# Performance work log

Measured on AMD Instinct MI355X. Metric: run time of the kernel, lower is better.

Reference implementation:

```python
import jax, jax.numpy as jnp
import numpy as np
import math

B, T, C = 8, 2048, 1024
N_LAYER, LAYER_ID = 24, 12


def setup_inputs() -> dict:
    key = jax.random.key(0)
    ks = jax.random.split(key, 8)
    # deterministic parameter init, mirroring RWKV_TimeMix.__init__
    ratio_0_to_1 = LAYER_ID / (N_LAYER - 1)
    ratio_1_to_almost0 = 1.0 - LAYER_ID / N_LAYER
    h = np.arange(C, dtype=np.float64)
    time_decay = (-5 + 8 * (h / (C - 1)) ** (0.7 + 1.3 * ratio_0_to_1)).astype(np.float32)
    zigzag = (np.array([(i + 1) % 3 - 1 for i in range(C)], dtype=np.float64) * 0.5)
    time_first = (np.ones(C) * math.log(0.3) + zigzag).astype(np.float32)
    xpos = (np.arange(C, dtype=np.float64) / C)
    time_mix_k = (xpos ** ratio_1_to_almost0).astype(np.float32).reshape(1, 1, C)
    time_mix_v = (xpos ** ratio_1_to_almost0 + 0.3 * ratio_0_to_1).astype(np.float32).reshape(1, 1, C)
    time_mix_r = (xpos ** (0.5 * ratio_1_to_almost0)).astype(np.float32).reshape(1, 1, C)
    scale = 1.0 / math.sqrt(C)
    return {
        "x": jax.random.normal(ks[0], (B, T, C), jnp.float32),
        "time_decay": jnp.asarray(time_decay),
        "time_first": jnp.asarray(time_first),
        "time_mix_k": jnp.asarray(time_mix_k),
        "time_mix_v": jnp.asarray(time_mix_v),
        "time_mix_r": jnp.asarray(time_mix_r),
        "Wk": jax.random.normal(ks[1], (C, C), jnp.float32) * scale,
        "Wv": jax.random.normal(ks[2], (C, C), jnp.float32) * scale,
        "Wr": jax.random.normal(ks[3], (C, C), jnp.float32) * scale,
        "Wo": jax.random.normal(ks[4], (C, C), jnp.float32) * scale,
    }


def wkv_scan(w_decay, u, k, v):
    """Numerically-stable RWKV-4 WKV recurrence.
    w_decay, u: [C]; k, v: [B, T, C]. Returns [B, T, C].
    """
    w = -jnp.exp(w_decay)  # negative decay per channel
    kt = jnp.swapaxes(k, 0, 1)  # [T, B, C]
    vt = jnp.swapaxes(v, 0, 1)
    Bn, Cn = k.shape[0], k.shape[2]
    aa0 = jnp.zeros((Bn, Cn), k.dtype)
    bb0 = jnp.zeros((Bn, Cn), k.dtype)
    pp0 = jnp.full((Bn, Cn), -1e38, k.dtype)

    def step(carry, kv):
        aa, bb, pp = carry
        k_t, v_t = kv
        ww = u + k_t
        q = jnp.maximum(pp, ww)
        e1 = jnp.exp(pp - q)
        e2 = jnp.exp(ww - q)
        y = (e1 * aa + e2 * v_t) / (e1 * bb + e2)
        ww2 = pp + w
        q2 = jnp.maximum(ww2, k_t)
        e1 = jnp.exp(ww2 - q2)
        e2 = jnp.exp(k_t - q2)
        return (e1 * aa + e2 * v_t, e1 * bb + e2, q2), y

    _, ys = jax.lax.scan(step, (aa0, bb0, pp0), (kt, vt))
    return jnp.swapaxes(ys, 0, 1)  # [B, T, C]


def reference(x, time_decay, time_first, time_mix_k, time_mix_v, time_mix_r, Wk, Wv, Wr, Wo):
    # time shift: x_{t-1}, zero at t=0
    xx = jnp.pad(x, ((0, 0), (1, 0), (0, 0)))[:, :-1]
    xk = x * time_mix_k + xx * (1.0 - time_mix_k)
    xv = x * time_mix_v + xx * (1.0 - time_mix_v)
    xr = x * time_mix_r + xx * (1.0 - time_mix_r)
    k = jnp.einsum("btc,oc->bto", xk, Wk)
    v = jnp.einsum("btc,oc->bto", xv, Wv)
    r = jnp.einsum("btc,oc->bto", xr, Wr)
    wkv = wkv_scan(time_decay, time_first, k, v)
    rwkv = jax.nn.sigmoid(r) * wkv
    return jnp.einsum("btc,oc->bto", rwkv, Wo)
```

## Files before the change

### kernel.cpp

```cpp
#include <hip/hip_runtime.h>

#define BB 8
#define TT 2048
#define CC 1024
#define WKV_L 32
#define WKV_NCH (TT / WKV_L)
#define WKV_LOG_NCH 6

typedef __bf16 bf16x8_t __attribute__((ext_vector_type(8)));
typedef float f32x4_t __attribute__((ext_vector_type(4)));

__device__ __forceinline__ unsigned short f2bf(float f) {
  unsigned u = __float_as_uint(f);
  u += 0x7fffu + ((u >> 16) & 1u);
  return (unsigned short)(u >> 16);
}
__device__ __forceinline__ float bf2f(unsigned short s) {
  return __uint_as_float(((unsigned)s) << 16);
}

#define GLOAD16(gp, lp)                                                        \
  __builtin_amdgcn_global_load_lds(                                            \
      (const __attribute__((address_space(1))) void*)(gp),                     \
      (__attribute__((address_space(3))) void*)(lp), 16, 0, 0)

__global__ __launch_bounds__(256) void mix3_cast_kernel(
    const float* __restrict__ x, const float* __restrict__ tmk,
    const float* __restrict__ tmv, const float* __restrict__ tmr,
    unsigned short* __restrict__ xk, unsigned short* __restrict__ xv,
    unsigned short* __restrict__ xr) {
  const size_t total4 = (size_t)BB * TT * CC / 4;
  for (size_t i = (size_t)blockIdx.x * blockDim.x + threadIdx.x; i < total4;
       i += (size_t)gridDim.x * blockDim.x) {
    size_t e = i * 4;
    int c = (int)(e & (CC - 1));
    int t = (int)((e / CC) & (TT - 1));
    float4 xv4 = ((const float4*)x)[i];
    float4 xp = make_float4(0.f, 0.f, 0.f, 0.f);
    if (t > 0) xp = ((const float4*)x)[i - CC / 4];
    float4 mk = *(const float4*)(tmk + c);
    float4 mv = *(const float4*)(tmv + c);
    float4 mr = *(const float4*)(tmr + c);
    ushort4 ok, ov, orr;
    ok.x = f2bf(xv4.x * mk.x + xp.x * (1.f - mk.x));
    ok.y = f2bf(xv4.y * mk.y + xp.y * (1.f - mk.y));
    ok.z = f2bf(xv4.z * mk.z + xp.z * (1.f - mk.z));
    ok.w = f2bf(xv4.w * mk.w + xp.w * (1.f - mk.w));
    ov.x = f2bf(xv4.x * mv.x + xp.x * (1.f - mv.x));
    ov.y = f2bf(xv4.y * mv.y + xp.y * (1.f - mv.y));
    ov.z = f2bf(xv4.z * mv.z + xp.z * (1.f - mv.z));
    ov.w = f2bf(xv4.w * mv.w + xp.w * (1.f - mv.w));
    orr.x = f2bf(xv4.x * mr.x + xp.x * (1.f - mr.x));
    orr.y = f2bf(xv4.y * mr.y + xp.y * (1.f - mr.y));
    orr.z = f2bf(xv4.z * mr.z + xp.z * (1.f - mr.z));
    orr.w = f2bf(xv4.w * mr.w + xp.w * (1.f - mr.w));
    *(ushort4*)(xk + e) = ok;
    *(ushort4*)(xv + e) = ov;
    *(ushort4*)(xr + e) = orr;
  }
}

__global__ __launch_bounds__(256) void cast_w4_kernel(
    const float* __restrict__ w0, const float* __restrict__ w1,
    const float* __restrict__ w2, const float* __restrict__ w3,
    unsigned short* __restrict__ o0, unsigned short* __restrict__ o1,
    unsigned short* __restrict__ o2, unsigned short* __restrict__ o3) {
  const int n4 = CC * CC / 4;
  for (int i = blockIdx.x * blockDim.x + threadIdx.x; i < 4 * n4;
       i += gridDim.x * blockDim.x) {
    int sel = i / n4;
    int j = i - sel * n4;
    const float* w = sel == 0 ? w0 : sel == 1 ? w1 : sel == 2 ? w2 : w3;
    unsigned short* o = sel == 0 ? o0 : sel == 1 ? o1 : sel == 2 ? o2 : o3;
    float4 v = ((const float4*)w)[j];
    ushort4 u;
    u.x = f2bf(v.x); u.y = f2bf(v.y); u.z = f2bf(v.z); u.w = f2bf(v.w);
    ((ushort4*)o)[j] = u;
  }
}

#define NT8 (CC / 64)

template <typename EPI>
__device__ __forceinline__ void gemm8_body(unsigned short* lds8,
                                           const unsigned short* __restrict__ A,
                                           const unsigned short* __restrict__ Bm,
                                           int tm, int tn, EPI epi) {
  const int tid = threadIdx.x;
  const int lane = tid & 63;
  const int wid = tid >> 6;
  const int wr = wid >> 2;
  const int wc = wid & 3;
  const int fr = lane & 15;
  const int fk = lane >> 4;

  const int srow = tid >> 3;
  const int gcol = (((tid & 7) ^ (srow & 7)) << 3);
  const unsigned short* Ag = A + (size_t)(tm * 256 + srow) * CC + gcol;
  const unsigned short* Bg = Bm + (size_t)(tn * 256 + srow) * CC + gcol;
  const int ldst = tid << 3;

  const int rowA = wr * 16 + fr;
  const int rowB = wc * 16 + fr;
  const int sx0 = ((fk ^ (fr & 7)) << 3);
  const int sx1 = (((4 + fk) ^ (fr & 7)) << 3);

  bf16x8_t aF[4][2];
  bf16x8_t bF[2][2][2];
  f32x4_t acc[8][4] = {};

#define STG_A(T, H)                                                            \
  {                                                                            \
    const unsigned short* g_ = Ag + (size_t)((H) * 128) * CC + (T) * 64;       \
    unsigned short* l_ = &lds8[(((T) & 1) << 14) + (H) * 8192 + ldst];         \
    GLOAD16(g_, l_);                                                           \
    GLOAD16(g_ + (size_t)64 * CC, l_ + 4096);                                  \
  }
#define STG_B(T, H)                                                            \
  {                                                                            \
    const unsigned short* g_ = Bg + (size_t)((H) * 128) * CC + (T) * 64;       \
    unsigned short* l_ = &lds8[32768 + (((T) & 1) << 14) + (H) * 8192 + ldst]; \
    GLOAD16(g_, l_);                                                           \
    GLOAD16(g_ + (size_t)64 * CC, l_ + 4096);                                  \
  }
#define LOADA(MH)                                                              \
  _Pragma("unroll") for (int i_ = 0; i_ < 4; ++i_) {                           \
    aF[i_][0] = *(const bf16x8_t*)&lds8[ab + ((MH) * 4 + i_) * 2048 + sx0];    \
    aF[i_][1] = *(const bf16x8_t*)&lds8[ab + ((MH) * 4 + i_) * 2048 + sx1];    \
  }
#define LOADB(NH)                                                              \
  _Pragma("unroll") for (int j_ = 0; j_ < 2; ++j_) {                           \
    bF[NH][j_][0] = *(const bf16x8_t*)&lds8[bb + ((NH) * 2 + j_) * 4096 + sx0];\
    bF[NH][j_][1] = *(const bf16x8_t*)&lds8[bb + ((NH) * 2 + j_) * 4096 + sx1];\
  }
#define MFMAQ(MH, NH)                                                          \
  _Pragma("unroll") for (int i_ = 0; i_ < 4; ++i_)                             \
  _Pragma("unroll") for (int j_ = 0; j_ < 2; ++j_) {                           \
    acc[(MH) * 4 + i_][(NH) * 2 + j_] = __builtin_amdgcn_mfma_f32_16x16x32_bf16( \
        aF[i_][0], bF[NH][j_][0], acc[(MH) * 4 + i_][(NH) * 2 + j_], 0, 0, 0); \
    acc[(MH) * 4 + i_][(NH) * 2 + j_] = __builtin_amdgcn_mfma_f32_16x16x32_bf16( \
        aF[i_][1], bF[NH][j_][1], acc[(MH) * 4 + i_][(NH) * 2 + j_], 0, 0, 0); \
  }

  STG_A(0, 0) STG_B(0, 0) STG_A(0, 1) STG_B(0, 1)
  STG_A(1, 0) STG_B(1, 0) STG_A(1, 1)
  asm volatile("s_waitcnt vmcnt(10)" ::: "memory");
  __builtin_amdgcn_s_barrier();

#pragma unroll
  for (int t = 0; t < NT8; ++t) {
    const int ab = ((t & 1) << 14) + rowA * 64;
    const int bb = 32768 + ((t & 1) << 14) + rowB * 64;
    LOADA(0) LOADB(0)
    if (t + 1 < NT8) { STG_B(t + 1, 1) }
    asm volatile("s_waitcnt vmcnt(8)" ::: "memory");
    __builtin_amdgcn_s_barrier();
    __builtin_amdgcn_s_setprio(1);
    MFMAQ(0, 0)
    __builtin_amdgcn_s_setprio(0);
    __builtin_amdgcn_s_barrier();
    LOADB(1)
    if (t + 2 < NT8) { STG_A(t + 2, 0) }
    __builtin_amdgcn_s_barrier();
    __builtin_amdgcn_s_setprio(1);
    MFMAQ(0, 1)
    __builtin_amdgcn_s_setprio(0);
    __builtin_amdgcn_s_barrier();
    LOADA(1)
    if (t + 2 < NT8) { STG_B(t + 2, 0) }
    __builtin_amdgcn_s_barrier();
    __builtin_amdgcn_s_setprio(1);
    MFMAQ(1, 0)
    __builtin_amdgcn_s_setprio(0);
    __builtin_amdgcn_s_barrier();
    if (t + 2 < NT8) { STG_A(t + 2, 1) }
    asm volatile("s_waitcnt vmcnt(10)" ::: "memory");
    __builtin_amdgcn_s_barrier();
    __builtin_amdgcn_s_setprio(1);
    MFMAQ(1, 1)
    __builtin_amdgcn_s_setprio(0);
    __builtin_amdgcn_s_barrier();
  }

#pragma unroll
  for (int im = 0; im < 8; ++im)
#pragma unroll
    for (int jn = 0; jn < 4; ++jn)
#pragma unroll
      for (int rg = 0; rg < 4; ++rg)
        epi((size_t)(tm * 256 + wr * 16 + im * 32 + (fk << 2) + rg) * CC +
                (size_t)(tn * 256 + wc * 16 + jn * 64 + fr),
            acc[im][jn][rg]);
#undef STG_A
#undef STG_B
#undef LOADA
#undef LOADB
#undef MFMAQ
}

template <int OUT_BF16>
__global__ __launch_bounds__(512, 2) void gemm8_one(const unsigned short* __restrict__ A,
                         const unsigned short* __restrict__ Bm,
                         void* __restrict__ Cm) {
  __shared__ unsigned short lds8[65536];
  int orig = blockIdx.x;
  int wg = (orig & 7) * 32 + (orig >> 3);
  int tm = wg >> 2;
  int tn = wg & 3;
  if (OUT_BF16)
    gemm8_body(lds8, A, Bm, tm, tn,
               [&](size_t off, float val) { ((unsigned short*)Cm)[off] = f2bf(val); });
  else
    gemm8_body(lds8, A, Bm, tm, tn,
               [&](size_t off, float val) { ((float*)Cm)[off] = val; });
}

__global__ __launch_bounds__(256) void wkv_phase1(const float* __restrict__ k,
                           const unsigned short* __restrict__ v,
                           const float* __restrict__ wdec,
                           float* __restrict__ Sa, float* __restrict__ Sb,
                           float* __restrict__ Sp) {
  int idx = blockIdx.x * blockDim.x + threadIdx.x;
  int c = idx & (CC - 1);
  int bj = idx >> 10;
  int j = bj & (WKV_NCH - 1);
  int b = bj >> WKV_LOG_NCH;
  float w = -__expf(wdec[c]);
  size_t base = ((size_t)b * TT + (size_t)j * WKV_L) * CC + c;
  float aa = 0.f, bb = 0.f, pp = -1e38f;
  for (int t = 0; t < WKV_L; ++t) {
    size_t off = base + (size_t)t * CC;
    float kt = k[off];
    float vt = bf2f(v[off]);
    pp += w;
    float d = kt - pp;
    if (d > 8.f) {
      float s = __expf(-d);
      aa *= s; bb *= s; pp = kt; d = 0.f;
    }
    float E = __expf(d);
    aa = fmaf(E, vt, aa);
    bb += E;
  }
  Sa[idx] = aa; Sb[idx] = bb; Sp[idx] = pp;
}

__global__ __launch_bounds__(256) void wkv_phase2(const float* __restrict__ wdec,
                           const float* __restrict__ Sa, const float* __restrict__ Sb,
                           const float* __restrict__ Sp,
                           float* __restrict__ Ia, float* __restrict__ Ib,
                           float* __restrict__ Ip) {
  int idx = blockIdx.x * blockDim.x + threadIdx.x;
  if (idx >= BB * CC) return;
  int c = idx & (CC - 1);
  int b = idx >> 10;
  float wL = -__expf(wdec[c]) * (float)WKV_L;
  float aa = 0.f, bb = 0.f, pp = -1e38f;
  for (int j = 0; j < WKV_NCH; ++j) {
    size_t s = (size_t)(b * WKV_NCH + j) * CC + c;
    Ia[s] = aa; Ib[s] = bb; Ip[s] = pp;
    float pd = pp + wL;
    float ps = Sp[s];
    float q = fmaxf(pd, ps);
    float e1 = __expf(pd - q);
    float e2 = __expf(ps - q);
    aa = fmaf(e1, aa, e2 * Sa[s]);
    bb = fmaf(e1, bb, e2 * Sb[s]);
    pp = q;
  }
}

__global__ __launch_bounds__(256) void wkv_phase3(const float* __restrict__ k,
                           const unsigned short* __restrict__ v,
                           const unsigned short* r,
                           const float* __restrict__ wdec,
                           const float* __restrict__ u,
                           const float* __restrict__ Ia, const float* __restrict__ Ib,
                           const float* __restrict__ Ip,
                           unsigned short* out) {
  int idx = blockIdx.x * blockDim.x + threadIdx.x;
  int c = idx & (CC - 1);
  int bj = idx >> 10;
  int j = bj & (WKV_NCH - 1);
  int b = bj >> WKV_LOG_NCH;
  float w = -__expf(wdec[c]);
  float uu = u[c];
  float aa = Ia[idx], bb = Ib[idx], pp = Ip[idx];
  size_t base = ((size_t)b * TT + (size_t)j * WKV_L) * CC + c;
  for (int t = 0; t < WKV_L; ++t) {
    size_t off = base + (size_t)t * CC;
    float kt = k[off];
    float vt = bf2f(v[off]);
    float dy = fminf(uu + kt - pp, 60.f);
    float Eu = __expf(dy);
    float y = fmaf(Eu, vt, aa) / (bb + Eu);
    float rt = bf2f(r[off]);
    float sr = 1.f / (1.f + __expf(-rt));
    out[off] = f2bf(sr * y);
    pp += w;
    float d = kt - pp;
    if (d > 8.f) {
      float s = __expf(-d);
      aa *= s; bb *= s; pp = kt; d = 0.f;
    }
    float E = __expf(d);
    aa = fmaf(E, vt, aa);
    bb += E;
  }
}

extern "C" void kernel_launch(void* const* d_in, const int* in_sizes, int n_in,
                              void* d_out, int out_size, void* d_ws, size_t ws_size,
                              hipStream_t stream) {
  const float* x    = (const float*)d_in[0];
  const float* tdec = (const float*)d_in[1];
  const float* tfir = (const float*)d_in[2];
  const float* tmk  = (const float*)d_in[3];
  const float* tmv  = (const float*)d_in[4];
  const float* tmr  = (const float*)d_in[5];
  const float* Wk   = (const float*)d_in[6];
  const float* Wv   = (const float*)d_in[7];
  const float* Wr   = (const float*)d_in[8];
  const float* Wo   = (const float*)d_in[9];

  const size_t M = (size_t)BB * TT;
  const size_t mixbytes = M * CC * 2;
  const size_t wbytes = (size_t)CC * CC * 2;
  const size_t nstate = (size_t)BB * WKV_NCH * CC;

  char* ws = (char*)d_ws;
  unsigned short* xkb = (unsigned short*)ws;  ws += mixbytes;
  unsigned short* xvb = (unsigned short*)ws;  ws += mixbytes;
  unsigned short* xrb = (unsigned short*)ws;  ws += mixbytes;
  unsigned short* rbuf = xkb;
  unsigned short* Wkb = (unsigned short*)ws; ws += wbytes;
  unsigned short* Wvb = (unsigned short*)ws; ws += wbytes;
  unsigned short* Wrb = (unsigned short*)ws; ws += wbytes;
  unsigned short* Wob = (unsigned short*)ws; ws += wbytes;
  float* kbuf = (float*)ws;                   ws += M * CC * 4;
  unsigned short* vbuf = (unsigned short*)ws; ws += mixbytes;
  float* Sa = (float*)ws; ws += nstate * 4;
  float* Sb = (float*)ws; ws += nstate * 4;
  float* Sp = (float*)ws; ws += nstate * 4;
  float* Ia = (float*)ws; ws += nstate * 4;
  float* Ib = (float*)ws; ws += nstate * 4;
  float* Ip = (float*)ws; ws += nstate * 4;

  dim3 blk(256);
  dim3 blk8(512);
  const int wkv_grid = (int)(nstate / 256);

  cast_w4_kernel<<<1024, blk, 0, stream>>>(Wk, Wv, Wr, Wo, Wkb, Wvb, Wrb, Wob);
  mix3_cast_kernel<<<2048, blk, 0, stream>>>(x, tmk, tmv, tmr, xkb, xvb, xrb);
  gemm8_one<0><<<256, blk8, 0, stream>>>(xkb, Wkb, kbuf);
  gemm8_one<1><<<256, blk8, 0, stream>>>(xvb, Wvb, vbuf);
  gemm8_one<1><<<256, blk8, 0, stream>>>(xrb, Wrb, rbuf);

  wkv_phase1<<<wkv_grid, blk, 0, stream>>>(kbuf, vbuf, tdec, Sa, Sb, Sp);
  wkv_phase2<<<(BB * CC + 255) / 256, blk, 0, stream>>>(tdec, Sa, Sb, Sp, Ia, Ib, Ip);
  wkv_phase3<<<wkv_grid, blk, 0, stream>>>(kbuf, vbuf, rbuf, tdec, tfir,
                                           Ia, Ib, Ip, rbuf);

  gemm8_one<0><<<256, blk8, 0, stream>>>(rbuf, Wob, d_out);
}
```

Baseline: 258.7 us.

## Batch K/V/R GEMMs into one launch, store k in bf16, vectorize WKV

Merges the three projection GEMMs into one grouped kernel with 768 workgroups so the CUs hold more concurrent blocks. It stores k as bf16 instead of fp32, which lowers memory traffic for the WKV phases. The WKV kernels now process two channels per thread with paired loads and stores, and the mixing kernel handles 8 elements per thread. The WKV state buffers reuse the no-longer-needed xk workspace. The trade-offs are less k precision and a possible wave-tail imbalance in the grouped GEMM.

```diff
diff --git a/kernel.cpp b/kernel.cpp
--- a/kernel.cpp
+++ b/kernel.cpp
@@ -9,6 +9,7 @@
 
 typedef __bf16 bf16x8_t __attribute__((ext_vector_type(8)));
 typedef float f32x4_t __attribute__((ext_vector_type(4)));
+typedef unsigned short ushort8_t __attribute__((ext_vector_type(8)));
 
 __device__ __forceinline__ unsigned short f2bf(float f) {
   unsigned u = __float_as_uint(f);
@@ -29,34 +30,41 @@
     const float* __restrict__ tmv, const float* __restrict__ tmr,
     unsigned short* __restrict__ xk, unsigned short* __restrict__ xv,
     unsigned short* __restrict__ xr) {
-  const size_t total4 = (size_t)BB * TT * CC / 4;
-  for (size_t i = (size_t)blockIdx.x * blockDim.x + threadIdx.x; i < total4;
+  const size_t total8 = (size_t)BB * TT * CC / 8;
+  for (size_t i = (size_t)blockIdx.x * blockDim.x + threadIdx.x; i < total8;
        i += (size_t)gridDim.x * blockDim.x) {
-    size_t e = i * 4;
+    size_t e = i * 8;
     int c = (int)(e & (CC - 1));
     int t = (int)((e / CC) & (TT - 1));
-    float4 xv4 = ((const float4*)x)[i];
-    float4 xp = make_float4(0.f, 0.f, 0.f, 0.f);
-    if (t > 0) xp = ((const float4*)x)[i - CC / 4];
-    float4 mk = *(const float4*)(tmk + c);
-    float4 mv = *(const float4*)(tmv + c);
-    float4 mr = *(const float4*)(tmr + c);
-    ushort4 ok, ov, orr;
-    ok.x = f2bf(xv4.x * mk.x + xp.x * (1.f - mk.x));
-    ok.y = f2bf(xv4.y * mk.y + xp.y * (1.f - mk.y));
-    ok.z = f2bf(xv4.z * mk.z + xp.z * (1.f - mk.z));
-    ok.w = f2bf(xv4.w * mk.w + xp.w * (1.f - mk.w));
-    ov.x = f2bf(xv4.x * mv.x + xp.x * (1.f - mv.x));
-    ov.y = f2bf(xv4.y * mv.y + xp.y * (1.f - mv.y));
-    ov.z = f2bf(xv4.z * mv.z + xp.z * (1.f - mv.z));
-    ov.w = f2bf(xv4.w * mv.w + xp.w * (1.f - mv.w));
-    orr.x = f2bf(xv4.x * mr.x + xp.x * (1.f - mr.x));
-    orr.y = f2bf(xv4.y * mr.y + xp.y * (1.f - mr.y));
-    orr.z = f2bf(xv4.z * mr.z + xp.z * (1.f - mr.z));
-    orr.w = f2bf(xv4.w * mr.w + xp.w * (1.f - mr.w));
-    *(ushort4*)(xk + e) = ok;
-    *(ushort4*)(xv + e) = ov;
-    *(ushort4*)(xr + e) = orr;
+    float4 xa = ((const float4*)x)[2 * i];
+    float4 xb = ((const float4*)x)[2 * i + 1];
+    float4 pa = make_float4(0.f, 0.f, 0.f, 0.f), pb = pa;
+    if (t > 0) {
+      pa = ((const float4*)x)[2 * i - 256];
+      pb = ((const float4*)x)[2 * i - 255];
+    }
+    float4 mka = *(const float4*)(tmk + c), mkb = *(const float4*)(tmk + c + 4);
+    float4 mva = *(const float4*)(tmv + c), mvb = *(const float4*)(tmv + c + 4);
+    float4 mra = *(const float4*)(tmr + c), mrb = *(const float4*)(tmr + c + 4);
+    ushort8_t ok, ov, orr;
+#define MIX1(dst, idx, xv_, pv_, m_)                                           \
+    dst[idx] = f2bf(xv_ * m_ + pv_ * (1.f - m_));
+    MIX1(ok, 0, xa.x, pa.x, mka.x) MIX1(ok, 1, xa.y, pa.y, mka.y)
+    MIX1(ok, 2, xa.z, pa.z, mka.z) MIX1(ok, 3, xa.w, pa.w, mka.w)
+    MIX1(ok, 4, xb.x, pb.x, mkb.x) MIX1(ok, 5, xb.y, pb.y, mkb.y)
+    MIX1(ok, 6, xb.z, pb.z, mkb.z) MIX1(ok, 7, xb.w, pb.w, mkb.w)
+    MIX1(ov, 0, xa.x, pa.x, mva.x) MIX1(ov, 1, xa.y, pa.y, mva.y)
+    MIX1(ov, 2, xa.z, pa.z, mva.z) MIX1(ov, 3, xa.w, pa.w, mva.w)
+    MIX1(ov, 4, xb.x, pb.x, mvb.x) MIX1(ov, 5, xb.y, pb.y, mvb.y)
+    MIX1(ov, 6, xb.z, pb.z, mvb.z) MIX1(ov, 7, xb.w, pb.w, mvb.w)
+    MIX1(orr, 0, xa.x, pa.x, mra.x) MIX1(orr, 1, xa.y, pa.y, mra.y)
+    MIX1(orr, 2, xa.z, pa.z, mra.z) MIX1(orr, 3, xa.w, pa.w, mra.w)
+    MIX1(orr, 4, xb.x, pb.x, mrb.x) MIX1(orr, 5, xb.y, pb.y, mrb.y)
+    MIX1(orr, 6, xb.z, pb.z, mrb.z) MIX1(orr, 7, xb.w, pb.w, mrb.w)
+#undef MIX1
+    *(ushort8_t*)(xk + e) = ok;
+    *(ushort8_t*)(xv + e) = ov;
+    *(ushort8_t*)(xr + e) = orr;
   }
 }
 
@@ -198,51 +206,70 @@
 #undef MFMAQ
 }
 
-template <int OUT_BF16>
+__global__ __launch_bounds__(512, 2) void gemm8_kvr(
+    const unsigned short* __restrict__ xk, const unsigned short* __restrict__ xv,
+    const unsigned short* __restrict__ xr, const unsigned short* __restrict__ Wk,
+    const unsigned short* __restrict__ Wv, const unsigned short* __restrict__ Wr,
+    unsigned short* __restrict__ kout, unsigned short* __restrict__ vout,
+    unsigned short* __restrict__ rout) {
+  __shared__ unsigned short lds8[65536];
+  int orig = blockIdx.x;
+  int wg = (orig & 7) * 96 + (orig >> 3);
+  int which = wg >> 8;
+  int rr = wg & 255;
+  int tm = rr >> 2;
+  int tn = rr & 3;
+  const unsigned short* A = which == 0 ? xk : which == 1 ? xv : xr;
+  const unsigned short* Bm = which == 0 ? Wk : which == 1 ? Wv : Wr;
+  unsigned short* o = which == 0 ? kout : which == 1 ? vout : rout;
+  gemm8_body(lds8, A, Bm, tm, tn,
+             [&](size_t off, float val) { o[off] = f2bf(val); });
+}
+
 __global__ __launch_bounds__(512, 2) void gemm8_one(const unsigned short* __restrict__ A,
                          const unsigned short* __restrict__ Bm,
-                         void* __restrict__ Cm) {
+                         float* __restrict__ Cm) {
   __shared__ unsigned short lds8[65536];
   int orig = blockIdx.x;
   int wg = (orig & 7) * 32 + (orig >> 3);
   int tm = wg >> 2;
   int tn = wg & 3;
-  if (OUT_BF16)
-    gemm8_body(lds8, A, Bm, tm, tn,
-               [&](size_t off, float val) { ((unsigned short*)Cm)[off] = f2bf(val); });
-  else
-    gemm8_body(lds8, A, Bm, tm, tn,
-               [&](size_t off, float val) { ((float*)Cm)[off] = val; });
-}
-
-__global__ __launch_bounds__(256) void wkv_phase1(const float* __restrict__ k,
+  gemm8_body(lds8, A, Bm, tm, tn,
+             [&](size_t off, float val) { Cm[off] = val; });
+}
+
+__global__ __launch_bounds__(256) void wkv_phase1(const unsigned short* __restrict__ k,
                            const unsigned short* __restrict__ v,
                            const float* __restrict__ wdec,
                            float* __restrict__ Sa, float* __restrict__ Sb,
                            float* __restrict__ Sp) {
   int idx = blockIdx.x * blockDim.x + threadIdx.x;
-  int c = idx & (CC - 1);
-  int bj = idx >> 10;
+  int c = (idx & (CC / 2 - 1)) << 1;
+  int bj = idx >> 9;
   int j = bj & (WKV_NCH - 1);
   int b = bj >> WKV_LOG_NCH;
-  float w = -__expf(wdec[c]);
+  float w0 = -__expf(wdec[c]), w1 = -__expf(wdec[c + 1]);
   size_t base = ((size_t)b * TT + (size_t)j * WKV_L) * CC + c;
-  float aa = 0.f, bb = 0.f, pp = -1e38f;
+  float aa0 = 0.f, bb0 = 0.f, pp0 = -1e38f;
+  float aa1 = 0.f, bb1 = 0.f, pp1 = -1e38f;
   for (int t = 0; t < WKV_L; ++t) {
     size_t off = base + (size_t)t * CC;
-    float kt = k[off];
-    float vt = bf2f(v[off]);
-    pp += w;
-    float d = kt - pp;
-    if (d > 8.f) {
-      float s = __expf(-d);
-      aa *= s; bb *= s; pp = kt; d = 0.f;
-    }
-    float E = __expf(d);
-    aa = fmaf(E, vt, aa);
-    bb += E;
-  }
-  Sa[idx] = aa; Sb[idx] = bb; Sp[idx] = pp;
+    ushort2 kk = *(const ushort2*)(k + off);
+    ushort2 vv = *(const ushort2*)(v + off);
+    float k0 = bf2f(kk.x), k1 = bf2f(kk.y);
+    float v0 = bf2f(vv.x), v1 = bf2f(vv.y);
+    pp0 += w0; pp1 += w1;
+    float d0 = k0 - pp0, d1 = k1 - pp1;
+    if (d0 > 8.f) { float s = __expf(-d0); aa0 *= s; bb0 *= s; pp0 = k0; d0 = 0.f; }
+    if (d1 > 8.f) { float s = __expf(-d1); aa1 *= s; bb1 *= s; pp1 = k1; d1 = 0.f; }
+    float E0 = __expf(d0), E1 = __expf(d1);
+    aa0 = fmaf(E0, v0, aa0); bb0 += E0;
+    aa1 = fmaf(E1, v1, aa1); bb1 += E1;
+  }
+  size_t s = (size_t)bj * CC + c;
+  *(float2*)(Sa + s) = make_float2(aa0, aa1);
+  *(float2*)(Sb + s) = make_float2(bb0, bb1);
+  *(float2*)(Sp + s) = make_float2(pp0, pp1);
 }
 
 __global__ __launch_bounds__(256) void wkv_phase2(const float* __restrict__ wdec,
@@ -270,7 +297,7 @@
   }
 }
 
-__global__ __launch_bounds__(256) void wkv_phase3(const float* __restrict__ k,
+__global__ __launch_bounds__(256) void wkv_phase3(const unsigned short* __restrict__ k,
                            const unsigned short* __restrict__ v,
                            const unsigned short* r,
                            const float* __restrict__ wdec,
@@ -279,33 +306,44 @@
                            const float* __restrict__ Ip,
                            unsigned short* out) {
   int idx = blockIdx.x * blockDim.x + threadIdx.x;
-  int c = idx & (CC - 1);
-  int bj = idx >> 10;
+  int c = (idx & (CC / 2 - 1)) << 1;
+  int bj = idx >> 9;
   int j = bj & (WKV_NCH - 1);
   int b = bj >> WKV_LOG_NCH;
-  float w = -__expf(wdec[c]);
-  float uu = u[c];
-  float aa = Ia[idx], bb = Ib[idx], pp = Ip[idx];
+  float w0 = -__expf(wdec[c]), w1 = -__expf(wdec[c + 1]);
+  float u0 = u[c], u1 = u[c + 1];
+  size_t st = (size_t)bj * CC + c;
+  float2 a2 = *(const float2*)(Ia + st);
+  float2 b2 = *(const float2*)(Ib + st);
+  float2 p2 = *(const float2*)(Ip + st);
+  float aa0 = a2.x, bb0 = b2.x, pp0 = p2.x;
+  float aa1 = a2.y, bb1 = b2.y, pp1 = p2.y;
   size_t base = ((size_t)b * TT + (size_t)j * WKV_L) * CC + c;
   for (int t = 0; t < WKV_L; ++t) {
     size_t off = base + (size_t)t * CC;
-    float kt = k[off];
-    float vt = bf2f(v[off]);
-    float dy = fminf(uu + kt - pp, 60.f);
-    float Eu = __expf(dy);
-    float y = fmaf(Eu, vt, aa) / (bb + Eu);
-    float rt = bf2f(r[off]);
-    float sr = 1.f / (1.f + __expf(-rt));
-    out[off] = f2bf(sr * y);
-    pp += w;
-    float d = kt - pp;
-    if (d > 8.f) {
-      float s = __expf(-d);
-      aa *= s; bb *= s; pp = kt; d = 0.f;
-    }
-    float E = __expf(d);
-    aa = fmaf(E, vt, aa);
-    bb += E;
+    ushort2 kk = *(const ushort2*)(k + off);
+    ushort2 vv = *(const ushort2*)(v + off);
+    ushort2 rr2 = *(const ushort2*)(r + off);
+    float k0 = bf2f(kk.x), k1 = bf2f(kk.y);
+    float v0 = bf2f(vv.x), v1 = bf2f(vv.y);
+    float dy0 = fminf(u0 + k0 - pp0, 60.f);
+    float dy1 = fminf(u1 + k1 - pp1, 60.f);
+    float Eu0 = __expf(dy0), Eu1 = __expf(dy1);
+    float y0 = fmaf(Eu0, v0, aa0) / (bb0 + Eu0);
+    float y1 = fmaf(Eu1, v1, aa1) / (bb1 + Eu1);
+    float sr0 = 1.f / (1.f + __expf(-bf2f(rr2.x)));
+    float sr1 = 1.f / (1.f + __expf(-bf2f(rr2.y)));
+    ushort2 o;
+    o.x = f2bf(sr0 * y0);
+    o.y = f2bf(sr1 * y1);
+    *(ushort2*)(out + off) = o;
+    pp0 += w0; pp1 += w1;
+    float d0 = k0 - pp0, d1 = k1 - pp1;
+    if (d0 > 8.f) { float s = __expf(-d0); aa0 *= s; bb0 *= s; pp0 = k0; d0 = 0.f; }
+    if (d1 > 8.f) { float s = __expf(-d1); aa1 *= s; bb1 *= s; pp1 = k1; d1 = 0.f; }
+    float E0 = __expf(d0), E1 = __expf(d1);
+    aa0 = fmaf(E0, v0, aa0); bb0 += E0;
+    aa1 = fmaf(E1, v1, aa1); bb1 += E1;
   }
 }
 
@@ -332,34 +370,34 @@
   unsigned short* xkb = (unsigned short*)ws;  ws += mixbytes;
   unsigned short* xvb = (unsigned short*)ws;  ws += mixbytes;
   unsigned short* xrb = (unsigned short*)ws;  ws += mixbytes;
-  unsigned short* rbuf = xkb;
   unsigned short* Wkb = (unsigned short*)ws; ws += wbytes;
   unsigned short* Wvb = (unsigned short*)ws; ws += wbytes;
   unsigned short* Wrb = (unsigned short*)ws; ws += wbytes;
   unsigned short* Wob = (unsigned short*)ws; ws += wbytes;
-  float* kbuf = (float*)ws;                   ws += M * CC * 4;
+  unsigned short* kbuf = (unsigned short*)ws; ws += mixbytes;
   unsigned short* vbuf = (unsigned short*)ws; ws += mixbytes;
-  float* Sa = (float*)ws; ws += nstate * 4;
-  float* Sb = (float*)ws; ws += nstate * 4;
-  float* Sp = (float*)ws; ws += nstate * 4;
-  float* Ia = (float*)ws; ws += nstate * 4;
-  float* Ib = (float*)ws; ws += nstate * 4;
-  float* Ip = (float*)ws; ws += nstate * 4;
+  unsigned short* rbuf = (unsigned short*)ws; ws += mixbytes;
+  char* so = (char*)xkb;
+  float* Sa = (float*)so; so += nstate * 4;
+  float* Sb = (float*)so; so += nstate * 4;
+  float* Sp = (float*)so; so += nstate * 4;
+  float* Ia = (float*)so; so += nstate * 4;
+  float* Ib = (float*)so; so += nstate * 4;
+  float* Ip = (float*)so; so += nstate * 4;
 
   dim3 blk(256);
   dim3 blk8(512);
-  const int wkv_grid = (int)(nstate / 256);
+  const int wkv_grid = (int)(nstate / 2 / 256);
 
   cast_w4_kernel<<<1024, blk, 0, stream>>>(Wk, Wv, Wr, Wo, Wkb, Wvb, Wrb, Wob);
   mix3_cast_kernel<<<2048, blk, 0, stream>>>(x, tmk, tmv, tmr, xkb, xvb, xrb);
-  gemm8_one<0><<<256, blk8, 0, stream>>>(xkb, Wkb, kbuf);
-  gemm8_one<1><<<256, blk8, 0, stream>>>(xvb, Wvb, vbuf);
-  gemm8_one<1><<<256, blk8, 0, stream>>>(xrb, Wrb, rbuf);
+  gemm8_kvr<<<768, blk8, 0, stream>>>(xkb, xvb, xrb, Wkb, Wvb, Wrb,
+                                      kbuf, vbuf, rbuf);
 
   wkv_phase1<<<wkv_grid, blk, 0, stream>>>(kbuf, vbuf, tdec, Sa, Sb, Sp);
   wkv_phase2<<<(BB * CC + 255) / 256, blk, 0, stream>>>(tdec, Sa, Sb, Sp, Ia, Ib, Ip);
   wkv_phase3<<<wkv_grid, blk, 0, stream>>>(kbuf, vbuf, rbuf, tdec, tfir,
                                            Ia, Ib, Ip, rbuf);
 
-  gemm8_one<0><<<256, blk8, 0, stream>>>(rbuf, Wob, d_out);
-}
+  gemm8_one<<<256, blk8, 0, stream>>>(rbuf, Wob, (float*)d_out);
+}
```

Result: faster. 250.0 us (-3.4%).
